# Kernel optimization log

Hardware: AMD Instinct MI355X
Metric: run time of the kernel (lower is better)

The kernel has to match this reference:

```python
import jax, jax.numpy as jnp
import numpy as np

DIM = 256
NH = 8
HD = DIM // NH          # 32
KD = HD // 2            # 16, attn_ratio=0.5
SCALE = KD ** -0.5
EPS = 1e-3              # BatchNorm2d eps=0.001
B, H, W = 8, 32, 32


def _bn(x, g, b, m, v):
    # inference-mode BatchNorm2d over channel axis 1 of NCHW
    inv = g / jnp.sqrt(v + EPS)
    return x * inv[None, :, None, None] + (b - m * inv)[None, :, None, None]


def setup_inputs() -> dict:
    key = jax.random.key(0)
    ks = jax.random.split(key, 16)
    h_out = DIM + 2 * NH * KD  # 512
    return {
        "x": jax.random.normal(ks[0], (B, DIM, H, W), jnp.float32),
        "qkv_w": jax.random.normal(ks[1], (h_out, DIM), jnp.float32) * 0.05,
        "qkv_g": jax.random.uniform(ks[2], (h_out,), jnp.float32, 0.5, 1.5),
        "qkv_b": jax.random.normal(ks[3], (h_out,), jnp.float32) * 0.1,
        "qkv_m": jax.random.normal(ks[4], (h_out,), jnp.float32) * 0.1,
        "qkv_v": jax.random.uniform(ks[5], (h_out,), jnp.float32, 0.5, 1.5),
        "pe_w": jax.random.normal(ks[6], (DIM, 1, 3, 3), jnp.float32) * 0.1,
        "pe_g": jax.random.uniform(ks[7], (DIM,), jnp.float32, 0.5, 1.5),
        "pe_b": jax.random.normal(ks[8], (DIM,), jnp.float32) * 0.1,
        "pe_m": jax.random.normal(ks[9], (DIM,), jnp.float32) * 0.1,
        "pe_v": jax.random.uniform(ks[10], (DIM,), jnp.float32, 0.5, 1.5),
        "proj_w": jax.random.normal(ks[11], (DIM, DIM), jnp.float32) * 0.05,
        "proj_g": jax.random.uniform(ks[12], (DIM,), jnp.float32, 0.5, 1.5),
        "proj_b": jax.random.normal(ks[13], (DIM,), jnp.float32) * 0.1,
        "proj_m": jax.random.normal(ks[14], (DIM,), jnp.float32) * 0.1,
        "proj_v": jax.random.uniform(ks[15], (DIM,), jnp.float32, 0.5, 1.5),
    }


def reference(x, qkv_w, qkv_g, qkv_b, qkv_m, qkv_v,
              pe_w, pe_g, pe_b, pe_m, pe_v,
              proj_w, proj_g, proj_b, proj_m, proj_v):
    b, c, h, w = x.shape
    n = h * w
    # qkv: 1x1 conv (no bias) + BN, act=Identity
    qkv = _bn(jnp.einsum('oc,bchw->bohw', qkv_w, x), qkv_g, qkv_b, qkv_m, qkv_v)
    qkv = qkv.reshape(b, NH, 2 * KD + HD, n)
    q, k, v = jnp.split(qkv, [KD, 2 * KD], axis=2)  # [b,nh,kd,n],[b,nh,kd,n],[b,nh,hd,n]
    # attn = q^T @ k * scale, softmax over keys (last dim)
    attn = jax.nn.softmax(jnp.einsum('bhkn,bhkm->bhnm', q, k) * SCALE, axis=-1)
    # v @ attn^T -> [b,nh,hd,n]
    out = jnp.einsum('bhdj,bhij->bhdi', v, attn).reshape(b, c, h, w)
    # depthwise 3x3 positional branch on v (reshaped to spatial)
    v_sp = v.reshape(b, c, h, w)
    pe = jax.lax.conv_general_dilated(v_sp, pe_w, window_strides=(1, 1),
                                      padding=((1, 1), (1, 1)),
                                      feature_group_count=c)
    pe = _bn(pe, pe_g, pe_b, pe_m, pe_v)
    x_attn = out + pe
    # final 1x1 projection + BN
    return _bn(jnp.einsum('oc,bchw->bohw', proj_w, x_attn),
               proj_g, proj_b, proj_m, proj_v)
```

## Files before the change

kernel.cpp:

```cpp
#include <hip/hip_runtime.h>
#include <hip/hip_bf16.h>

#define B_    8
#define DIM_  256
#define NH_   8
#define HD_   32
#define KD_   16
#define HOUT_ 512
#define N_    1024
#define SCALE_ 0.25f
#define EPS_  1e-3f

typedef unsigned short u16;
typedef __attribute__((ext_vector_type(8))) short short8;
typedef __attribute__((ext_vector_type(4))) float f32x4;

union H4 { uint2 u; u16 e[4]; };

__device__ __forceinline__ float b2f(u16 u) {
    union { unsigned int i; float f; } c;
    c.i = ((unsigned int)u) << 16;
    return c.f;
}

__device__ __forceinline__ u16 f2b(float f) {
    union { float f; unsigned int i; } c;
    c.f = f;
    unsigned int x = c.i;
    return (u16)((x + 0x7fffu + ((x >> 16) & 1u)) >> 16);
}

__global__ __launch_bounds__(256) void k_prep(
    const float* __restrict__ qw, const float* __restrict__ pw,
    const float* __restrict__ pew,
    const float* __restrict__ qg, const float* __restrict__ qb,
    const float* __restrict__ qm, const float* __restrict__ qv,
    const float* __restrict__ pg, const float* __restrict__ pb,
    const float* __restrict__ pm, const float* __restrict__ pv,
    const float* __restrict__ eg, const float* __restrict__ eb,
    const float* __restrict__ em, const float* __restrict__ ev,
    u16* __restrict__ wq_bf, u16* __restrict__ wp_bf,
    float2* __restrict__ bnq, float2* __restrict__ bnp,
    float* __restrict__ wpe, float* __restrict__ bnpe)
{
    int i = blockIdx.x * 256 + threadIdx.x;
    wq_bf[i] = f2b(qw[i]);
    if (i < 65536) wp_bf[i] = f2b(pw[i]);
    if (i < 512) {
        float inv = qg[i] / sqrtf(qv[i] + EPS_);
        bnq[i] = make_float2(inv, qb[i] - qm[i] * inv);
    } else if (i < 768) {
        int o = i - 512;
        float inv = pg[o] / sqrtf(pv[o] + EPS_);
        bnp[o] = make_float2(inv, pb[o] - pm[o] * inv);
    }
    if (i < 2304) {
        int c = i / 9;
        float inv = eg[c] / sqrtf(ev[c] + EPS_);
        wpe[i] = pew[i] * inv;
        if (i % 9 == 0) bnpe[c] = eb[c] - em[c] * inv;
    }
}

__global__ __launch_bounds__(256) void k_xt(
    const float* __restrict__ x, u16* __restrict__ xT)
{
    __shared__ float t_s[64][65];
    int blk = blockIdx.x;
    int nt = blk & 15, ct = (blk >> 4) & 3, b = blk >> 6;
    int t = threadIdx.x;
    int c0 = ct * 64, n0 = nt * 64;
    #pragma unroll
    for (int i = 0; i < 16; ++i) {
        int idx = i * 256 + t;
        int c = idx >> 6, n = idx & 63;
        t_s[n][c] = x[(size_t)(b * DIM_ + c0 + c) * N_ + n0 + n];
    }
    __syncthreads();
    #pragma unroll
    for (int i = 0; i < 16; ++i) {
        int idx = i * 256 + t;
        int n = idx >> 6, c = idx & 63;
        xT[(size_t)(b * N_ + n0 + n) * DIM_ + c0 + c] = f2b(t_s[n][c]);
    }
}

__global__ __launch_bounds__(256) void k_qkv(
    const u16* __restrict__ xT, const u16* __restrict__ wbf,
    const float2* __restrict__ bn, u16* __restrict__ qkv)
{
    int blk = blockIdx.x;
    int nb = blk & 7, ob = (blk >> 3) & 7, b = blk >> 6;
    int t = threadIdx.x;
    int wv_ = t >> 6, lane = t & 63, quad = lane >> 4, l16 = lane & 15;
    int o_base = ob * 64 + (wv_ & 1) * 32;
    int n_base = nb * 128 + (wv_ >> 1) * 64;

    f32x4 acc[2][4];
    #pragma unroll
    for (int ot = 0; ot < 2; ++ot)
        #pragma unroll
        for (int nt = 0; nt < 4; ++nt) acc[ot][nt] = (f32x4){0.f, 0.f, 0.f, 0.f};

    const u16* xb = xT + (size_t)b * N_ * DIM_;
    for (int c0 = 0; c0 < DIM_; c0 += 32) {
        short8 af[2];
        #pragma unroll
        for (int ot = 0; ot < 2; ++ot)
            af[ot] = *(const short8*)(wbf + (size_t)(o_base + ot * 16 + l16) * DIM_ + c0 + quad * 8);
        short8 bf[4];
        #pragma unroll
        for (int nt = 0; nt < 4; ++nt)
            bf[nt] = *(const short8*)(xb + (size_t)(n_base + nt * 16 + l16) * DIM_ + c0 + quad * 8);
        #pragma unroll
        for (int ot = 0; ot < 2; ++ot)
            #pragma unroll
            for (int nt = 0; nt < 4; ++nt)
                acc[ot][nt] = __builtin_amdgcn_mfma_f32_16x16x32_bf16(af[ot], bf[nt], acc[ot][nt], 0, 0, 0);
    }
    #pragma unroll
    for (int ot = 0; ot < 2; ++ot)
        #pragma unroll
        for (int r = 0; r < 4; ++r) {
            int o = o_base + ot * 16 + quad * 4 + r;
            float2 ib = bn[o];
            u16* dst = qkv + (size_t)(b * HOUT_ + o) * N_ + n_base + l16;
            #pragma unroll
            for (int nt = 0; nt < 4; ++nt)
                dst[nt * 16] = f2b(acc[ot][nt][r] * ib.x + ib.y);
        }
}

struct MainSmem { u16 k_t[256][24]; u16 p_s[4][16][80]; };
union  SmemU    { MainSmem m; float v_pe[128][33]; };

__global__ __launch_bounds__(256) void k_attn(
    const u16* __restrict__ qkv, const float* __restrict__ wpe,
    const float* __restrict__ bnpe, u16* __restrict__ xattnT)
{
    __shared__ SmemU su;
    __shared__ u16   q_t[64][24];
    __shared__ float o_s[4][32][17];

    int blk = blockIdx.x;
    int qb = blk & 15;
    int h  = (blk >> 4) & 7;
    int b  = blk >> 7;
    int t    = threadIdx.x;
    int wv_  = t >> 6;
    int lane = t & 63;
    int quad = lane >> 4;
    int l16  = lane & 15;
    const u16* base = qkv + (size_t)(b * HOUT_ + h * 64) * N_;

    {
        int q = t & 63, d4 = (t >> 6) * 4;
        H4 hh;
        #pragma unroll
        for (int i = 0; i < 4; ++i)
            hh.e[i] = f2b(b2f(base[(size_t)(d4 + i) * N_ + qb * 64 + q]) * SCALE_);
        *(uint2*)&q_t[q][d4] = hh.u;
    }
    __syncthreads();

    short8 qf = {0, 0, 0, 0, 0, 0, 0, 0};
    if (quad < 2) qf = *(const short8*)&q_t[wv_ * 16 + l16][quad * 8];

    f32x4 oa0 = {0.f, 0.f, 0.f, 0.f};
    f32x4 oa1 = {0.f, 0.f, 0.f, 0.f};
    float l_acc[4] = {0.f, 0.f, 0.f, 0.f};

    for (int ch = 0; ch < 4; ++ch) {
        int ch0 = ch * 256;
        __syncthreads();
        {
            #pragma unroll
            for (int d4 = 0; d4 < 16; d4 += 4) {
                H4 hh;
                #pragma unroll
                for (int i = 0; i < 4; ++i)
                    hh.e[i] = base[(size_t)(16 + d4 + i) * N_ + ch0 + t];
                *(uint2*)&su.m.k_t[t][d4] = hh.u;
            }
        }
        __syncthreads();

        for (int kt = 0; kt < 4; ++kt) {
            int key0 = ch0 + kt * 64;
            #pragma unroll
            for (int nt = 0; nt < 4; ++nt) {
                short8 kf = {0, 0, 0, 0, 0, 0, 0, 0};
                if (quad < 2) kf = *(const short8*)&su.m.k_t[kt * 64 + nt * 16 + l16][quad * 8];
                f32x4 zero = {0.f, 0.f, 0.f, 0.f};
                f32x4 s = __builtin_amdgcn_mfma_f32_16x16x32_bf16(qf, kf, zero, 0, 0, 0);
                #pragma unroll
                for (int r = 0; r < 4; ++r) {
                    float p = __expf(fminf(s[r], 80.f));
                    l_acc[r] += p;
                    su.m.p_s[wv_][quad * 4 + r][nt * 16 + l16] = f2b(p);
                }
            }
            #pragma unroll
            for (int kc = 0; kc < 2; ++kc) {
                short8 pf = *(const short8*)&su.m.p_s[wv_][l16][kc * 32 + quad * 8];
                {
                    const u16* vsrc = base + (size_t)(32 + l16) * N_ + key0 + kc * 32 + quad * 8;
                    oa0 = __builtin_amdgcn_mfma_f32_16x16x32_bf16(pf, *(const short8*)vsrc, oa0, 0, 0, 0);
                }
                {
                    const u16* vsrc = base + (size_t)(48 + l16) * N_ + key0 + kc * 32 + quad * 8;
                    oa1 = __builtin_amdgcn_mfma_f32_16x16x32_bf16(pf, *(const short8*)vsrc, oa1, 0, 0, 0);
                }
            }
        }
    }

    #pragma unroll
    for (int r = 0; r < 4; ++r) {
        float v = l_acc[r];
        v += __shfl_xor(v, 1);
        v += __shfl_xor(v, 2);
        v += __shfl_xor(v, 4);
        v += __shfl_xor(v, 8);
        l_acc[r] = v;
    }
    #pragma unroll
    for (int r = 0; r < 4; ++r) {
        o_s[wv_][l16][quad * 4 + r]      = oa0[r] / l_acc[r];
        o_s[wv_][16 + l16][quad * 4 + r] = oa1[r] / l_acc[r];
    }
    __syncthreads();

    {
        int ybase = qb * 2 - 1;
        #pragma unroll
        for (int i = 0; i < 16; ++i) {
            int idx = i * 256 + t;
            int d = idx >> 7, px = idx & 127;
            int y = ybase + (px >> 5);
            float v = 0.f;
            if (y >= 0 && y < 32)
                v = b2f(base[(size_t)(32 + d) * N_ + y * 32 + (px & 31)]);
            su.v_pe[px][d] = v;
        }
    }
    __syncthreads();

    {
        int d = t & 31, pxg = t >> 5;
        int c = h * 32 + d;
        float w9[9];
        #pragma unroll
        for (int k = 0; k < 9; ++k) w9[k] = wpe[c * 9 + k];
        float beta = bnpe[c];
        #pragma unroll
        for (int ii = 0; ii < 8; ++ii) {
            int pl = pxg * 8 + ii;
            int xx0 = pl & 31;
            float s = beta;
            #pragma unroll
            for (int dy = -1; dy <= 1; ++dy) {
                #pragma unroll
                for (int dx = -1; dx <= 1; ++dx) {
                    int xx = xx0 + dx;
                    if (xx < 0 || xx > 31) continue;
                    s += w9[(dy + 1) * 3 + (dx + 1)] * su.v_pe[pl + 32 + dy * 32 + dx][d];
                }
            }
            float o = o_s[pl >> 4][d][pl & 15];
            xattnT[(size_t)(b * N_ + qb * 64 + pl) * DIM_ + c] = f2b(o + s);
        }
    }
}

__global__ __launch_bounds__(256) void k_proj(
    const u16* __restrict__ xattnT, const u16* __restrict__ wbf,
    const float2* __restrict__ bn, float* __restrict__ out)
{
    int blk = blockIdx.x;
    int nb = blk & 7, ob = (blk >> 3) & 3, b = blk >> 5;
    int t = threadIdx.x;
    int wv_ = t >> 6, lane = t & 63, quad = lane >> 4, l16 = lane & 15;
    int o_base = ob * 64 + (wv_ & 1) * 32;
    int n_base = nb * 128 + (wv_ >> 1) * 64;

    f32x4 acc[2][4];
    #pragma unroll
    for (int ot = 0; ot < 2; ++ot)
        #pragma unroll
        for (int nt = 0; nt < 4; ++nt) acc[ot][nt] = (f32x4){0.f, 0.f, 0.f, 0.f};

    const u16* xb = xattnT + (size_t)b * N_ * DIM_;
    for (int c0 = 0; c0 < DIM_; c0 += 32) {
        short8 af[2];
        #pragma unroll
        for (int ot = 0; ot < 2; ++ot)
            af[ot] = *(const short8*)(wbf + (size_t)(o_base + ot * 16 + l16) * DIM_ + c0 + quad * 8);
        short8 bf[4];
        #pragma unroll
        for (int nt = 0; nt < 4; ++nt)
            bf[nt] = *(const short8*)(xb + (size_t)(n_base + nt * 16 + l16) * DIM_ + c0 + quad * 8);
        #pragma unroll
        for (int ot = 0; ot < 2; ++ot)
            #pragma unroll
            for (int nt = 0; nt < 4; ++nt)
                acc[ot][nt] = __builtin_amdgcn_mfma_f32_16x16x32_bf16(af[ot], bf[nt], acc[ot][nt], 0, 0, 0);
    }
    #pragma unroll
    for (int ot = 0; ot < 2; ++ot)
        #pragma unroll
        for (int r = 0; r < 4; ++r) {
            int o = o_base + ot * 16 + quad * 4 + r;
            float2 ib = bn[o];
            float* dst = out + (size_t)(b * DIM_ + o) * N_ + n_base + l16;
            #pragma unroll
            for (int nt = 0; nt < 4; ++nt)
                dst[nt * 16] = acc[ot][nt][r] * ib.x + ib.y;
        }
}

extern "C" void kernel_launch(void* const* d_in, const int* in_sizes, int n_in,
                              void* d_out, int out_size, void* d_ws, size_t ws_size,
                              hipStream_t stream)
{
    const float* x      = (const float*)d_in[0];
    const float* qkv_w  = (const float*)d_in[1];
    const float* qkv_g  = (const float*)d_in[2];
    const float* qkv_b  = (const float*)d_in[3];
    const float* qkv_m  = (const float*)d_in[4];
    const float* qkv_v  = (const float*)d_in[5];
    const float* pe_w   = (const float*)d_in[6];
    const float* pe_g   = (const float*)d_in[7];
    const float* pe_b   = (const float*)d_in[8];
    const float* pe_m   = (const float*)d_in[9];
    const float* pe_v   = (const float*)d_in[10];
    const float* proj_w = (const float*)d_in[11];
    const float* proj_g = (const float*)d_in[12];
    const float* proj_b = (const float*)d_in[13];
    const float* proj_m = (const float*)d_in[14];
    const float* proj_v = (const float*)d_in[15];
    float* out = (float*)d_out;

    char* p = (char*)d_ws;
    u16*    qkv    = (u16*)p;    p += (size_t)B_ * HOUT_ * N_ * sizeof(u16);
    u16*    xT     = (u16*)p;    p += (size_t)B_ * N_ * DIM_ * sizeof(u16);
    u16*    xattnT = (u16*)p;    p += (size_t)B_ * N_ * DIM_ * sizeof(u16);
    u16*    wq_bf  = (u16*)p;    p += (size_t)HOUT_ * DIM_ * sizeof(u16);
    u16*    wp_bf  = (u16*)p;    p += (size_t)DIM_ * DIM_ * sizeof(u16);
    float2* bnq    = (float2*)p; p += 512 * sizeof(float2);
    float2* bnp    = (float2*)p; p += 256 * sizeof(float2);
    float*  wpe    = (float*)p;  p += 2304 * sizeof(float);
    float*  bnpe   = (float*)p;

    hipLaunchKernelGGL(k_prep, dim3(512), dim3(256), 0, stream,
                       qkv_w, proj_w, pe_w,
                       qkv_g, qkv_b, qkv_m, qkv_v,
                       proj_g, proj_b, proj_m, proj_v,
                       pe_g, pe_b, pe_m, pe_v,
                       wq_bf, wp_bf, bnq, bnp, wpe, bnpe);
    hipLaunchKernelGGL(k_xt, dim3(512), dim3(256), 0, stream, x, xT);
    hipLaunchKernelGGL(k_qkv, dim3(512), dim3(256), 0, stream,
                       xT, wq_bf, bnq, qkv);
    hipLaunchKernelGGL(k_attn, dim3(B_ * NH_ * 16), dim3(256), 0, stream,
                       qkv, wpe, bnpe, xattnT);
    hipLaunchKernelGGL(k_proj, dim3(256), dim3(256), 0, stream,
                       xattnT, wp_bf, bnp, out);
}
```

Baseline: 159.5 us.

## Compute transposed scores so P feeds PV MFMA from registers, skipping LDS

Computes S^T = K·Q^T with MFMA so each lane's accumulator holds four keys for one query. Those values are exponentiated and packed straight into the B operand of a 16x16x16 bf16 MFMA against V. This removes the LDS round trip for the probability tile and the p_s shared buffer. The cost is twice as many, smaller PV MFMAs, and the path only activates if the compiler exposes the _1k builtin.

Measured after the change: 184.3 us. 1.16x slower.

```diff
diff --git a/kernel.cpp b/kernel.cpp
--- a/kernel.cpp
+++ b/kernel.cpp
@@ -11,8 +11,15 @@
 #define SCALE_ 0.25f
 #define EPS_  1e-3f
 
+#if __has_builtin(__builtin_amdgcn_mfma_f32_16x16x16bf16_1k)
+#define USE_1K 1
+#else
+#define USE_1K 0
+#endif
+
 typedef unsigned short u16;
 typedef __attribute__((ext_vector_type(8))) short short8;
+typedef __attribute__((ext_vector_type(4))) short short4b;
 typedef __attribute__((ext_vector_type(4))) float f32x4;
 
 union H4 { uint2 u; u16 e[4]; };
@@ -131,7 +138,11 @@
         }
 }
 
+#if USE_1K
+struct MainSmem { u16 k_t[256][24]; };
+#else
 struct MainSmem { u16 k_t[256][24]; u16 p_s[4][16][80]; };
+#endif
 union  SmemU    { MainSmem m; float v_pe[128][33]; };
 
 __global__ __launch_bounds__(256) void k_attn(
@@ -166,6 +177,56 @@
     short8 qf = {0, 0, 0, 0, 0, 0, 0, 0};
     if (quad < 2) qf = *(const short8*)&q_t[wv_ * 16 + l16][quad * 8];
 
+#if USE_1K
+    f32x4 oaT0 = {0.f, 0.f, 0.f, 0.f};
+    f32x4 oaT1 = {0.f, 0.f, 0.f, 0.f};
+    float l_part = 0.f;
+
+    for (int ch = 0; ch < 4; ++ch) {
+        int ch0 = ch * 256;
+        __syncthreads();
+        {
+            #pragma unroll
+            for (int d4 = 0; d4 < 16; d4 += 4) {
+                H4 hh;
+                #pragma unroll
+                for (int i = 0; i < 4; ++i)
+                    hh.e[i] = base[(size_t)(16 + d4 + i) * N_ + ch0 + t];
+                *(uint2*)&su.m.k_t[t][d4] = hh.u;
+            }
+        }
+        __syncthreads();
+
+        #pragma unroll 4
+        for (int kt = 0; kt < 16; ++kt) {
+            int key0 = ch0 + kt * 16;
+            short8 kf = {0, 0, 0, 0, 0, 0, 0, 0};
+            if (quad < 2) kf = *(const short8*)&su.m.k_t[kt * 16 + l16][quad * 8];
+            f32x4 zero = {0.f, 0.f, 0.f, 0.f};
+            f32x4 sT = __builtin_amdgcn_mfma_f32_16x16x32_bf16(kf, qf, zero, 0, 0, 0);
+            short4b pb;
+            #pragma unroll
+            for (int r = 0; r < 4; ++r) {
+                float p = __expf(fminf(sT[r], 80.f));
+                l_part += p;
+                pb[r] = f2b(p);
+            }
+            short4b vf0 = *(const short4b*)(base + (size_t)(32 + l16) * N_ + key0 + quad * 4);
+            oaT0 = __builtin_amdgcn_mfma_f32_16x16x16bf16_1k(vf0, pb, oaT0, 0, 0, 0);
+            short4b vf1 = *(const short4b*)(base + (size_t)(48 + l16) * N_ + key0 + quad * 4);
+            oaT1 = __builtin_amdgcn_mfma_f32_16x16x16bf16_1k(vf1, pb, oaT1, 0, 0, 0);
+        }
+    }
+
+    l_part += __shfl_xor(l_part, 16);
+    l_part += __shfl_xor(l_part, 32);
+    float linv = 1.f / fmaxf(l_part, 1e-30f);
+    #pragma unroll
+    for (int r = 0; r < 4; ++r) {
+        o_s[wv_][quad * 4 + r][l16]      = oaT0[r] * linv;
+        o_s[wv_][16 + quad * 4 + r][l16] = oaT1[r] * linv;
+    }
+#else
     f32x4 oa0 = {0.f, 0.f, 0.f, 0.f};
     f32x4 oa1 = {0.f, 0.f, 0.f, 0.f};
     float l_acc[4] = {0.f, 0.f, 0.f, 0.f};
@@ -214,7 +275,6 @@
             }
         }
     }
-
     #pragma unroll
     for (int r = 0; r < 4; ++r) {
         float v = l_acc[r];
@@ -229,6 +289,7 @@
         o_s[wv_][l16][quad * 4 + r]      = oa0[r] / l_acc[r];
         o_s[wv_][16 + l16][quad * 4 + r] = oa1[r] / l_acc[r];
     }
+#endif
     __syncthreads();
 
     {
```

## Restructure attention to keep P in registers via transposed MFMA, 128 queries per block

Applied to the files above, without the earlier changes.

The attention kernel now computes S^T = K·Q^T so each lane's softmax probabilities land directly in the B-operand layout of a 16x16x16 MFMA against V. This removes the LDS round trip for P. Each block now handles 128 queries (two 16-query tiles per wave), which halves the grid and reuses every K/V load for twice as many queries. The output staging buffer is switched to bf16 and the positional-encoding halo load is adapted to the larger tile. Separately, the weight-prep and x-transpose kernels are merged into a single launch, which risks some load imbalance between block types.

Measured after the change: 153.0 us. 4.1% less time.

```diff
diff --git a/kernel.cpp b/kernel.cpp
--- a/kernel.cpp
+++ b/kernel.cpp
@@ -13,6 +13,7 @@
 
 typedef unsigned short u16;
 typedef __attribute__((ext_vector_type(8))) short short8;
+typedef __attribute__((ext_vector_type(4))) short short4b;
 typedef __attribute__((ext_vector_type(4))) float f32x4;
 
 union H4 { uint2 u; u16 e[4]; };
@@ -30,7 +31,8 @@
     return (u16)((x + 0x7fffu + ((x >> 16) & 1u)) >> 16);
 }
 
-__global__ __launch_bounds__(256) void k_prep(
+__global__ __launch_bounds__(256) void k_pre(
+    const float* __restrict__ x, u16* __restrict__ xT,
     const float* __restrict__ qw, const float* __restrict__ pw,
     const float* __restrict__ pew,
     const float* __restrict__ qg, const float* __restrict__ qb,
@@ -43,32 +45,30 @@
     float2* __restrict__ bnq, float2* __restrict__ bnp,
     float* __restrict__ wpe, float* __restrict__ bnpe)
 {
-    int i = blockIdx.x * 256 + threadIdx.x;
-    wq_bf[i] = f2b(qw[i]);
-    if (i < 65536) wp_bf[i] = f2b(pw[i]);
-    if (i < 512) {
-        float inv = qg[i] / sqrtf(qv[i] + EPS_);
-        bnq[i] = make_float2(inv, qb[i] - qm[i] * inv);
-    } else if (i < 768) {
-        int o = i - 512;
-        float inv = pg[o] / sqrtf(pv[o] + EPS_);
-        bnp[o] = make_float2(inv, pb[o] - pm[o] * inv);
-    }
-    if (i < 2304) {
-        int c = i / 9;
-        float inv = eg[c] / sqrtf(ev[c] + EPS_);
-        wpe[i] = pew[i] * inv;
-        if (i % 9 == 0) bnpe[c] = eb[c] - em[c] * inv;
-    }
-}
-
-__global__ __launch_bounds__(256) void k_xt(
-    const float* __restrict__ x, u16* __restrict__ xT)
-{
     __shared__ float t_s[64][65];
     int blk = blockIdx.x;
+    int t = threadIdx.x;
+    if (blk >= 512) {
+        int i = (blk - 512) * 256 + t;
+        wq_bf[i] = f2b(qw[i]);
+        if (i < 65536) wp_bf[i] = f2b(pw[i]);
+        if (i < 512) {
+            float inv = qg[i] / sqrtf(qv[i] + EPS_);
+            bnq[i] = make_float2(inv, qb[i] - qm[i] * inv);
+        } else if (i < 768) {
+            int o = i - 512;
+            float inv = pg[o] / sqrtf(pv[o] + EPS_);
+            bnp[o] = make_float2(inv, pb[o] - pm[o] * inv);
+        }
+        if (i < 2304) {
+            int c = i / 9;
+            float inv = eg[c] / sqrtf(ev[c] + EPS_);
+            wpe[i] = pew[i] * inv;
+            if (i % 9 == 0) bnpe[c] = eb[c] - em[c] * inv;
+        }
+        return;
+    }
     int nt = blk & 15, ct = (blk >> 4) & 3, b = blk >> 6;
-    int t = threadIdx.x;
     int c0 = ct * 64, n0 = nt * 64;
     #pragma unroll
     for (int i = 0; i < 16; ++i) {
@@ -131,44 +131,56 @@
         }
 }
 
-struct MainSmem { u16 k_t[256][24]; u16 p_s[4][16][80]; };
-union  SmemU    { MainSmem m; float v_pe[128][33]; };
+struct MainS { u16 q_t[128][24]; u16 k_t[256][24]; };
+union  SmemU { MainS m; float v_pe[192][33]; };
 
 __global__ __launch_bounds__(256) void k_attn(
     const u16* __restrict__ qkv, const float* __restrict__ wpe,
     const float* __restrict__ bnpe, u16* __restrict__ xattnT)
 {
     __shared__ SmemU su;
-    __shared__ u16   q_t[64][24];
-    __shared__ float o_s[4][32][17];
+    __shared__ u16 o_s[4][32][34];
 
     int blk = blockIdx.x;
-    int qb = blk & 15;
-    int h  = (blk >> 4) & 7;
-    int b  = blk >> 7;
+    int qc = blk & 7;
+    int h  = (blk >> 3) & 7;
+    int b  = blk >> 6;
     int t    = threadIdx.x;
     int wv_  = t >> 6;
     int lane = t & 63;
     int quad = lane >> 4;
     int l16  = lane & 15;
     const u16* base = qkv + (size_t)(b * HOUT_ + h * 64) * N_;
+    int q0g = qc * 128;
 
     {
-        int q = t & 63, d4 = (t >> 6) * 4;
-        H4 hh;
+        int q = t & 127, dh = (t >> 7) * 8;
+        H4 a, c4;
         #pragma unroll
         for (int i = 0; i < 4; ++i)
-            hh.e[i] = f2b(b2f(base[(size_t)(d4 + i) * N_ + qb * 64 + q]) * SCALE_);
-        *(uint2*)&q_t[q][d4] = hh.u;
+            a.e[i]  = f2b(b2f(base[(size_t)(dh + i) * N_ + q0g + q]) * SCALE_);
+        #pragma unroll
+        for (int i = 0; i < 4; ++i)
+            c4.e[i] = f2b(b2f(base[(size_t)(dh + 4 + i) * N_ + q0g + q]) * SCALE_);
+        *(uint2*)&su.m.q_t[q][dh]     = a.u;
+        *(uint2*)&su.m.q_t[q][dh + 4] = c4.u;
     }
     __syncthreads();
 
-    short8 qf = {0, 0, 0, 0, 0, 0, 0, 0};
-    if (quad < 2) qf = *(const short8*)&q_t[wv_ * 16 + l16][quad * 8];
-
-    f32x4 oa0 = {0.f, 0.f, 0.f, 0.f};
-    f32x4 oa1 = {0.f, 0.f, 0.f, 0.f};
-    float l_acc[4] = {0.f, 0.f, 0.f, 0.f};
+    short8 qf[2];
+    #pragma unroll
+    for (int qt = 0; qt < 2; ++qt) {
+        qf[qt] = (short8){0, 0, 0, 0, 0, 0, 0, 0};
+        if (quad < 2)
+            qf[qt] = *(const short8*)&su.m.q_t[wv_ * 32 + qt * 16 + l16][quad * 8];
+    }
+
+    f32x4 oa[2][2];
+    #pragma unroll
+    for (int qt = 0; qt < 2; ++qt)
+        #pragma unroll
+        for (int dh = 0; dh < 2; ++dh) oa[qt][dh] = (f32x4){0.f, 0.f, 0.f, 0.f};
+    float lp[2] = {0.f, 0.f};
 
     for (int ch = 0; ch < 4; ++ch) {
         int ch0 = ch * 256;
@@ -185,63 +197,64 @@
         }
         __syncthreads();
 
-        for (int kt = 0; kt < 4; ++kt) {
-            int key0 = ch0 + kt * 64;
-            #pragma unroll
-            for (int nt = 0; nt < 4; ++nt) {
-                short8 kf = {0, 0, 0, 0, 0, 0, 0, 0};
-                if (quad < 2) kf = *(const short8*)&su.m.k_t[kt * 64 + nt * 16 + l16][quad * 8];
-                f32x4 zero = {0.f, 0.f, 0.f, 0.f};
-                f32x4 s = __builtin_amdgcn_mfma_f32_16x16x32_bf16(qf, kf, zero, 0, 0, 0);
-                #pragma unroll
-                for (int r = 0; r < 4; ++r) {
-                    float p = __expf(fminf(s[r], 80.f));
-                    l_acc[r] += p;
-                    su.m.p_s[wv_][quad * 4 + r][nt * 16 + l16] = f2b(p);
-                }
-            }
-            #pragma unroll
-            for (int kc = 0; kc < 2; ++kc) {
-                short8 pf = *(const short8*)&su.m.p_s[wv_][l16][kc * 32 + quad * 8];
-                {
-                    const u16* vsrc = base + (size_t)(32 + l16) * N_ + key0 + kc * 32 + quad * 8;
-                    oa0 = __builtin_amdgcn_mfma_f32_16x16x32_bf16(pf, *(const short8*)vsrc, oa0, 0, 0, 0);
-                }
-                {
-                    const u16* vsrc = base + (size_t)(48 + l16) * N_ + key0 + kc * 32 + quad * 8;
-                    oa1 = __builtin_amdgcn_mfma_f32_16x16x32_bf16(pf, *(const short8*)vsrc, oa1, 0, 0, 0);
-                }
-            }
-        }
-    }
-
-    #pragma unroll
-    for (int r = 0; r < 4; ++r) {
-        float v = l_acc[r];
-        v += __shfl_xor(v, 1);
-        v += __shfl_xor(v, 2);
-        v += __shfl_xor(v, 4);
-        v += __shfl_xor(v, 8);
-        l_acc[r] = v;
-    }
-    #pragma unroll
-    for (int r = 0; r < 4; ++r) {
-        o_s[wv_][l16][quad * 4 + r]      = oa0[r] / l_acc[r];
-        o_s[wv_][16 + l16][quad * 4 + r] = oa1[r] / l_acc[r];
+        #pragma unroll 4
+        for (int kt = 0; kt < 16; ++kt) {
+            int key0 = ch0 + kt * 16;
+            short8 kf = {0, 0, 0, 0, 0, 0, 0, 0};
+            if (quad < 2) kf = *(const short8*)&su.m.k_t[kt * 16 + l16][quad * 8];
+            f32x4 zero = {0.f, 0.f, 0.f, 0.f};
+            f32x4 sT0 = __builtin_amdgcn_mfma_f32_16x16x32_bf16(kf, qf[0], zero, 0, 0, 0);
+            f32x4 sT1 = __builtin_amdgcn_mfma_f32_16x16x32_bf16(kf, qf[1], zero, 0, 0, 0);
+            short4b vf0 = *(const short4b*)(base + (size_t)(32 + l16) * N_ + key0 + quad * 4);
+            short4b vf1 = *(const short4b*)(base + (size_t)(48 + l16) * N_ + key0 + quad * 4);
+            short4b pb0, pb1;
+            #pragma unroll
+            for (int r = 0; r < 4; ++r) {
+                float p = __expf(fminf(sT0[r], 80.f));
+                lp[0] += p;
+                pb0[r] = f2b(p);
+            }
+            #pragma unroll
+            for (int r = 0; r < 4; ++r) {
+                float p = __expf(fminf(sT1[r], 80.f));
+                lp[1] += p;
+                pb1[r] = f2b(p);
+            }
+            oa[0][0] = __builtin_amdgcn_mfma_f32_16x16x16bf16_1k(vf0, pb0, oa[0][0], 0, 0, 0);
+            oa[0][1] = __builtin_amdgcn_mfma_f32_16x16x16bf16_1k(vf1, pb0, oa[0][1], 0, 0, 0);
+            oa[1][0] = __builtin_amdgcn_mfma_f32_16x16x16bf16_1k(vf0, pb1, oa[1][0], 0, 0, 0);
+            oa[1][1] = __builtin_amdgcn_mfma_f32_16x16x16bf16_1k(vf1, pb1, oa[1][1], 0, 0, 0);
+        }
+    }
+
+    #pragma unroll
+    for (int qt = 0; qt < 2; ++qt) {
+        float v = lp[qt];
+        v += __shfl_xor(v, 16);
+        v += __shfl_xor(v, 32);
+        float linv = 1.f / fmaxf(v, 1e-30f);
+        #pragma unroll
+        for (int dh = 0; dh < 2; ++dh)
+            #pragma unroll
+            for (int r = 0; r < 4; ++r)
+                o_s[wv_][dh * 16 + quad * 4 + r][qt * 16 + l16] = f2b(oa[qt][dh][r] * linv);
     }
     __syncthreads();
 
     {
-        int ybase = qb * 2 - 1;
-        #pragma unroll
-        for (int i = 0; i < 16; ++i) {
-            int idx = i * 256 + t;
-            int d = idx >> 7, px = idx & 127;
-            int y = ybase + (px >> 5);
-            float v = 0.f;
-            if (y >= 0 && y < 32)
-                v = b2f(base[(size_t)(32 + d) * N_ + y * 32 + (px & 31)]);
-            su.v_pe[px][d] = v;
+        int ybase = qc * 4 - 1;
+        int px = t & 31, dg = t >> 5;
+        #pragma unroll
+        for (int j = 0; j < 6; ++j) {
+            int y = ybase + j;
+            #pragma unroll
+            for (int s = 0; s < 4; ++s) {
+                int d = dg + s * 8;
+                float v = 0.f;
+                if (y >= 0 && y < 32)
+                    v = b2f(base[(size_t)(32 + d) * N_ + y * 32 + px]);
+                su.v_pe[j * 32 + px][d] = v;
+            }
         }
     }
     __syncthreads();
@@ -254,8 +267,8 @@
         for (int k = 0; k < 9; ++k) w9[k] = wpe[c * 9 + k];
         float beta = bnpe[c];
         #pragma unroll
-        for (int ii = 0; ii < 8; ++ii) {
-            int pl = pxg * 8 + ii;
+        for (int ii = 0; ii < 16; ++ii) {
+            int pl = pxg * 16 + ii;
             int xx0 = pl & 31;
             float s = beta;
             #pragma unroll
@@ -267,8 +280,8 @@
                     s += w9[(dy + 1) * 3 + (dx + 1)] * su.v_pe[pl + 32 + dy * 32 + dx][d];
                 }
             }
-            float o = o_s[pl >> 4][d][pl & 15];
-            xattnT[(size_t)(b * N_ + qb * 64 + pl) * DIM_ + c] = f2b(o + s);
+            float o = b2f(o_s[pl >> 5][d][pl & 31]);
+            xattnT[(size_t)(b * N_ + q0g + pl) * DIM_ + c] = f2b(o + s);
         }
     }
 }
@@ -352,16 +365,15 @@
     float*  wpe    = (float*)p;  p += 2304 * sizeof(float);
     float*  bnpe   = (float*)p;
 
-    hipLaunchKernelGGL(k_prep, dim3(512), dim3(256), 0, stream,
-                       qkv_w, proj_w, pe_w,
+    hipLaunchKernelGGL(k_pre, dim3(1024), dim3(256), 0, stream,
+                       x, xT, qkv_w, proj_w, pe_w,
                        qkv_g, qkv_b, qkv_m, qkv_v,
                        proj_g, proj_b, proj_m, proj_v,
                        pe_g, pe_b, pe_m, pe_v,
                        wq_bf, wp_bf, bnq, bnp, wpe, bnpe);
-    hipLaunchKernelGGL(k_xt, dim3(512), dim3(256), 0, stream, x, xT);
     hipLaunchKernelGGL(k_qkv, dim3(512), dim3(256), 0, stream,
                        xT, wq_bf, bnq, qkv);
-    hipLaunchKernelGGL(k_attn, dim3(B_ * NH_ * 16), dim3(256), 0, stream,
+    hipLaunchKernelGGL(k_attn, dim3(512), dim3(256), 0, stream,
                        qkv, wpe, bnpe, xattnT);
     hipLaunchKernelGGL(k_proj, dim3(256), dim3(256), 0, stream,
                        xattnT, wp_bf, bnp, out);
```
